# Kernel optimization log

Measured on AMD Instinct MI355X. Metric: run time of the kernel, lower is better.

Reference implementation:

```python
import jax, jax.numpy as jnp
import numpy as np

N_NODES = 50000
N_EDGES = 800000
NODE_FEAT = 3
EDGE_FEAT = 2
EMBED = 64
HIDDEN = 128
LAYERS = 4
POLY = 8


def setup_inputs() -> dict:
    key = jax.random.key(0)
    ks = jax.random.split(key, 24)
    s = 0.05
    inp = {
        "node_features": jax.random.normal(ks[0], (N_NODES, NODE_FEAT), jnp.float32),
        "edge_index": jax.random.randint(ks[1], (2, N_EDGES), 0, N_NODES, jnp.int32),
        "edge_features": jax.random.normal(ks[2], (N_EDGES, EDGE_FEAT), jnp.float32),
        "n": N_NODES,
        # node encoder MLP
        "enc_w1": jax.random.normal(ks[3], (NODE_FEAT, HIDDEN), jnp.float32) * s,
        "enc_b1": jnp.zeros((HIDDEN,), jnp.float32),
        "enc_w2": jax.random.normal(ks[4], (HIDDEN, EMBED), jnp.float32) * s,
        "enc_b2": jnp.zeros((EMBED,), jnp.float32),
        # per-layer conv message MLP (stacked over layers)
        "conv_w1": jax.random.normal(ks[5], (LAYERS, 2 * EMBED + EDGE_FEAT, EMBED), jnp.float32) * s,
        "conv_b1": jnp.zeros((LAYERS, EMBED), jnp.float32),
        "conv_w2": jax.random.normal(ks[6], (LAYERS, EMBED, EMBED), jnp.float32) * s,
        "conv_b2": jnp.zeros((LAYERS, EMBED), jnp.float32),
        # per-layer skip linear and layernorm
        "skip_w": jax.random.normal(ks[7], (LAYERS, EMBED, EMBED), jnp.float32) * s,
        "skip_b": jnp.zeros((LAYERS, EMBED), jnp.float32),
        "ln_g": jnp.ones((LAYERS, EMBED), jnp.float32),
        "ln_b": jnp.zeros((LAYERS, EMBED), jnp.float32),
        # polynomial head
        "head_w1": jax.random.normal(ks[8], (EMBED, EMBED), jnp.float32) * s,
        "head_b1": jnp.zeros((EMBED,), jnp.float32),
        "head_w2": jnp.zeros((EMBED, POLY), jnp.float32),  # zero-init per module
        "head_b2": jnp.ones((POLY,), jnp.float32),         # bias filled with 1.0
    }
    return inp


def _layernorm(x, g, b, eps=1e-5):
    mu = jnp.mean(x, axis=-1, keepdims=True)
    var = jnp.var(x, axis=-1, keepdims=True)
    return (x - mu) * jax.lax.rsqrt(var + eps) * g + b


def reference(node_features, edge_index, edge_features, n,
              enc_w1, enc_b1, enc_w2, enc_b2,
              conv_w1, conv_b1, conv_w2, conv_b2,
              skip_w, skip_b, ln_g, ln_b,
              head_w1, head_b1, head_w2, head_b2):
    rows, cols = edge_index[0], edge_index[1]
    # node encoder
    h = jax.nn.relu(node_features @ enc_w1 + enc_b1) @ enc_w2 + enc_b2  # [n, E]
    L = conv_w1.shape[0]
    for i in range(L):
        # gather + concat: [E_edges, 2*embed + edge_feat]
        msg_in = jnp.concatenate([h[rows], h[cols], edge_features], axis=-1)
        msg = jax.nn.relu(msg_in @ conv_w1[i] + conv_b1[i]) @ conv_w2[i] + conv_b2[i]
        agg = jax.ops.segment_sum(msg, rows, num_segments=n)  # scatter_add over source rows
        h_new = agg + h @ skip_w[i] + skip_b[i]
        h = jax.nn.relu(_layernorm(h_new, ln_g[i], ln_b[i]))
    # polynomial head
    return jax.nn.relu(h @ head_w1 + head_b1) @ head_w2 + head_b2  # [n, poly_degree]
```

## Files before the change

kernel.cpp:

```cpp
#include <hip/hip_runtime.h>

typedef unsigned short u16;
typedef __attribute__((ext_vector_type(8))) short bf16x8;
typedef __attribute__((ext_vector_type(4))) float f32x4;

#define MFMA16(a,b,c) __builtin_amdgcn_mfma_f32_16x16x32_bf16((a),(b),(c),0,0,0)

static __device__ __forceinline__ u16 f2bf(float x){
    unsigned int u = __float_as_uint(x);
    u += 0x7FFFu + ((u >> 16) & 1u);
    return (u16)(u >> 16);
}
static __device__ __forceinline__ float bf2f(short s){
    return __uint_as_float(((unsigned int)(u16)s) << 16);
}

static __device__ __forceinline__ bf16x8 load_bfrag(const float* __restrict__ W, int ldn, int n, int k0){
    bf16x8 r;
    #pragma unroll
    for (int j = 0; j < 8; ++j) r[j] = (short)f2bf(W[(k0 + j) * ldn + n]);
    return r;
}

__global__ __launch_bounds__(256) void enc_kernel(
    const float* __restrict__ X, const float* __restrict__ W1, const float* __restrict__ B1,
    const float* __restrict__ W2, const float* __restrict__ B2,
    const float* __restrict__ cW1, const float* __restrict__ cB1,
    u16* __restrict__ hbf, u16* __restrict__ Ubf, u16* __restrict__ Vbf, int N)
{
    __shared__ u16 sHid[64 * 136];
    __shared__ u16 sH[64 * 72];
    const int tid = threadIdx.x;
    const int w = tid >> 6, l = tid & 63, l15 = l & 15, quad = l >> 4;

    bf16x8 bW[4][4];
    #pragma unroll
    for (int ks = 0; ks < 4; ++ks)
        #pragma unroll
        for (int f = 0; f < 4; ++f)
            bW[ks][f] = load_bfrag(W2, 64, f * 16 + l15, ks * 32 + quad * 8);
    float b2v[4];
    #pragma unroll
    for (int f = 0; f < 4; ++f) b2v[f] = B2[f * 16 + l15];

    const int nbase = blockIdx.x * 64 + w * 16;

    {
        int e = l >> 2;
        int node = nbase + e; if (node > N - 1) node = N - 1;
        float x0 = X[node * 3], x1 = X[node * 3 + 1], x2 = X[node * 3 + 2];
        int k0 = (l & 3) * 32;
        u16* dst = sHid + (w * 16 + e) * 136 + k0;
        #pragma unroll
        for (int j = 0; j < 32; ++j){
            int k = k0 + j;
            float hv = x0 * W1[k] + x1 * W1[128 + k] + x2 * W1[256 + k] + B1[k];
            dst[j] = f2bf(hv > 0.f ? hv : 0.f);
        }
    }

    f32x4 acc[4];
    #pragma unroll
    for (int f = 0; f < 4; ++f){ acc[f][0]=b2v[f]; acc[f][1]=b2v[f]; acc[f][2]=b2v[f]; acc[f][3]=b2v[f]; }
    #pragma unroll
    for (int ks = 0; ks < 4; ++ks){
        bf16x8 a = *(const bf16x8*)&sHid[(w * 16 + l15) * 136 + ks * 32 + quad * 8];
        #pragma unroll
        for (int f = 0; f < 4; ++f) acc[f] = MFMA16(a, bW[ks][f], acc[f]);
    }
    #pragma unroll
    for (int r = 0; r < 4; ++r){
        int node = nbase + quad * 4 + r;
        #pragma unroll
        for (int f = 0; f < 4; ++f){
            u16 hb = f2bf(acc[f][r]);
            sH[(w * 16 + quad * 4 + r) * 72 + f * 16 + l15] = hb;
            if (node < N) hbf[(size_t)node * 64 + f * 16 + l15] = hb;
        }
    }

    bf16x8 bA[2][4], bB[2][4];
    #pragma unroll
    for (int kk = 0; kk < 2; ++kk)
        #pragma unroll
        for (int f = 0; f < 4; ++f){
            int n = f * 16 + l15, k0 = kk * 32 + quad * 8;
            bA[kk][f] = load_bfrag(cW1,           64, n, k0);
            bB[kk][f] = load_bfrag(cW1 + 64 * 64, 64, n, k0);
        }
    float b1n[4];
    #pragma unroll
    for (int f = 0; f < 4; ++f) b1n[f] = cB1[f * 16 + l15];

    bf16x8 a0 = *(const bf16x8*)&sH[(w * 16 + l15) * 72 + quad * 8];
    bf16x8 a1 = *(const bf16x8*)&sH[(w * 16 + l15) * 72 + 32 + quad * 8];

    f32x4 ua[4], va[4];
    #pragma unroll
    for (int f = 0; f < 4; ++f){
        ua[f][0]=b1n[f]; ua[f][1]=b1n[f]; ua[f][2]=b1n[f]; ua[f][3]=b1n[f];
        va[f][0]=0.f; va[f][1]=0.f; va[f][2]=0.f; va[f][3]=0.f;
    }
    #pragma unroll
    for (int f = 0; f < 4; ++f){ ua[f] = MFMA16(a0, bA[0][f], ua[f]); va[f] = MFMA16(a0, bB[0][f], va[f]); }
    #pragma unroll
    for (int f = 0; f < 4; ++f){ ua[f] = MFMA16(a1, bA[1][f], ua[f]); va[f] = MFMA16(a1, bB[1][f], va[f]); }

    #pragma unroll
    for (int r = 0; r < 4; ++r){
        int node = nbase + quad * 4 + r;
        if (node < N){
            #pragma unroll
            for (int f = 0; f < 4; ++f){
                Ubf[(size_t)node * 64 + f * 16 + l15] = f2bf(ua[f][r]);
                Vbf[(size_t)node * 64 + f * 16 + l15] = f2bf(va[f][r]);
            }
        }
    }
}

__global__ __launch_bounds__(256) void countB_kernel(const int* __restrict__ rows,
                                                     int* __restrict__ countsB, int E, int NB){
    __shared__ int c[1024];
    for (int i = threadIdx.x; i < NB; i += 256) c[i] = 0;
    __syncthreads();
    for (int i = blockIdx.x * 256 + threadIdx.x; i < E; i += gridDim.x * 256)
        atomicAdd(&c[rows[i] >> 6], 1);
    __syncthreads();
    for (int i = threadIdx.x; i < NB; i += 256){
        int v = c[i];
        if (v) atomicAdd(&countsB[i], v);
    }
}

__global__ __launch_bounds__(1024) void scanB_kernel(const int* __restrict__ countsB,
                                                     int* __restrict__ offsets,
                                                     int* __restrict__ cursorB, int NB){
    __shared__ int sc[1024];
    const int tid = threadIdx.x;
    int x = (tid < NB) ? countsB[tid] : 0;
    sc[tid] = x;
    __syncthreads();
    for (int d = 1; d < 1024; d <<= 1){
        int v = (tid >= d) ? sc[tid - d] : 0;
        __syncthreads();
        sc[tid] += v;
        __syncthreads();
    }
    int excl = sc[tid] - x;
    if (tid < NB){ offsets[tid] = excl; cursorB[tid] = excl; }
    if (tid == NB - 1) offsets[NB] = sc[tid];
}

#define CHUNK 8192

__global__ __launch_bounds__(1024) void binpack_kernel(
    const int* __restrict__ rows, const int* __restrict__ cols,
    const float* __restrict__ EF, int* __restrict__ cursorB,
    uint2* __restrict__ erec, int E)
{
    __shared__ u16 sRow[CHUNK];
    __shared__ u16 sPerm[CHUNK];
    __shared__ int cntA[1024], cntE[1024], cntC[1024], baseB[1024], sc[1024];
    const int tid = threadIdx.x;
    const int cbase = blockIdx.x * CHUNK;
    int C = E - cbase; if (C > CHUNK) C = CHUNK;
    if (C <= 0) return;

    cntA[tid] = 0;
    __syncthreads();
    for (int k = tid; k < C; k += 1024){
        int r = rows[cbase + k];
        sRow[k] = (u16)r;
        atomicAdd(&cntA[r >> 6], 1);
    }
    __syncthreads();
    sc[tid] = cntA[tid];
    __syncthreads();
    for (int d = 1; d < 1024; d <<= 1){
        int v = (tid >= d) ? sc[tid - d] : 0;
        __syncthreads();
        sc[tid] += v;
        __syncthreads();
    }
    int excl = sc[tid] - cntA[tid];
    cntE[tid] = excl;
    cntC[tid] = excl;
    if (cntA[tid] > 0) baseB[tid] = atomicAdd(&cursorB[tid], cntA[tid]);
    __syncthreads();
    for (int k = tid; k < C; k += 1024){
        int b = sRow[k] >> 6;
        int p = atomicAdd(&cntC[b], 1);
        sPerm[p] = (u16)k;
    }
    __syncthreads();
    for (int p = tid; p < C; p += 1024){
        int k = sPerm[p];
        int i = cbase + k;
        int r = sRow[k];
        int b = r >> 6;
        float2 ef = *(const float2*)&EF[2 * i];
        uint2 v;
        v.x = (unsigned)r | ((unsigned)cols[i] << 16);
        v.y = (unsigned)f2bf(ef.x) | ((unsigned)f2bf(ef.y) << 16);
        erec[baseB[b] + (p - cntE[b])] = v;
    }
}

#define ISSUE_UV(recv, U0, U1, V0, V1) do {                                  \
    int rr_ = (int)((recv).x & 0xFFFFu); if (rr_ == 0xFFFF) rr_ = 0;         \
    int cc_ = (int)((recv).x >> 16);                                         \
    const u16* pu_ = Ubf + (size_t)rr_ * 64 + quad * 8;                      \
    const u16* pv_ = Vbf + (size_t)cc_ * 64 + quad * 8;                      \
    U0 = *(const bf16x8*)(pu_);                                              \
    U1 = *(const bf16x8*)(pu_ + 32);                                         \
    V0 = *(const bf16x8*)(pv_);                                              \
    V1 = *(const bf16x8*)(pv_ + 32);                                         \
} while (0)

static __device__ __forceinline__ unsigned cvtpk(float a, float b){
    unsigned d;
    asm("v_cvt_pk_bf16_f32 %0, %1, %2" : "=v"(d) : "v"(a), "v"(b));
    return d;
}
#define PACK8(dst, x) do {                                                   \
    union { bf16x8 v; unsigned int d[4]; } _u;                               \
    _u.d[0] = cvtpk(x[0], x[1]); _u.d[1] = cvtpk(x[2], x[3]);                \
    _u.d[2] = cvtpk(x[4], x[5]); _u.d[3] = cvtpk(x[6], x[7]);                \
    dst = _u.v;                                                              \
} while (0)

__global__ __launch_bounds__(256, 3) void fused_kernel(
    const u16* __restrict__ Ubf, const u16* __restrict__ Vbf,
    const uint2* __restrict__ erec, const int* __restrict__ offsets,
    const float* __restrict__ W1,
    const float* __restrict__ W2, const float* __restrict__ B2,
    u16* __restrict__ hbf,
    const float* __restrict__ SW, const float* __restrict__ SB,
    const float* __restrict__ LG, const float* __restrict__ LB,
    const float* __restrict__ cW1, const float* __restrict__ cB1,
    u16* __restrict__ Un, u16* __restrict__ Vn,
    int N)
{
    __shared__ u16 sMsgT[2][64 * 72];
    __shared__ u16 sRowT[2][64];
    __shared__ u16 sH[64 * 72];
    const int tid = threadIdx.x;
    const int w = tid >> 6, l = tid & 63, l15 = l & 15, quad = l >> 4;
    const int w16 = w * 16;

    bf16x8 bW2[2][4];
    #pragma unroll
    for (int kk = 0; kk < 2; ++kk)
        #pragma unroll
        for (int f = 0; f < 4; ++f)
            bW2[kk][f] = load_bfrag(W2, 64, f * 16 + l15, kk * 32 + quad * 8);
    float bias2[4];
    #pragma unroll
    for (int f = 0; f < 4; ++f) bias2[f] = B2[f * 16 + l15];

    const float* Wc0 = W1 + 128 * 64;
    const float* Wc1 = W1 + 129 * 64;
    float e0l[8], e0h[8], e1l[8], e1h[8];
    #pragma unroll
    for (int j = 0; j < 8; ++j){
        int kl = quad * 8 + j;
        e0l[j] = Wc0[kl];       e0h[j] = Wc0[32 + kl];
        e1l[j] = Wc1[kl];       e1h[j] = Wc1[32 + kl];
    }

    const int b = blockIdx.x;
    const int start = offsets[b], end = offsets[b + 1];
    const int nt = (end - start + 63) >> 6;
    const int tgtrow = w16 + l15;

    f32x4 aggC[4] = {};

    auto LOADREC = [&](int t) -> uint2 {
        int e = start + t * 64 + w16 + l15;
        if (e < end) return erec[e];
        uint2 s; s.x = 0x0000FFFFu; s.y = 0u; return s;
    };

    if (nt > 0){
        uint2 recA = LOADREC(0);
        uint2 recB = (nt > 1) ? LOADREC(1) : recA;
        bf16x8 u0, u1, v0, v1;
        ISSUE_UV(recA, u0, u1, v0, v1);

        for (int t = 0; t < nt; ++t){
            uint2 recC = LOADREC(t + 2 < nt ? t + 2 : nt - 1);
            bf16x8 nu0, nu1, nv0, nv1;
            ISSUE_UV(recB, nu0, nu1, nv0, nv1);

            int rn_raw = (int)(recA.x & 0xFFFFu);
            float ef0 = bf2f((short)(recA.y & 0xFFFFu));
            float ef1 = bf2f((short)(recA.y >> 16));

            float xl[8], xh[8];
            #pragma unroll
            for (int j = 0; j < 8; ++j){
                float hA = fmaf(ef1, e1l[j], ef0 * e0l[j]);
                float hB = fmaf(ef1, e1h[j], ef0 * e0h[j]);
                xl[j] = fmaxf(hA + bf2f(u0[j]) + bf2f(v0[j]), 0.f);
                xh[j] = fmaxf(hB + bf2f(u1[j]) + bf2f(v1[j]), 0.f);
            }
            bf16x8 a0, a1;
            PACK8(a0, xl);
            PACK8(a1, xh);

            f32x4 m[4];
            #pragma unroll
            for (int f = 0; f < 4; ++f){ m[f][0]=bias2[f]; m[f][1]=bias2[f]; m[f][2]=bias2[f]; m[f][3]=bias2[f]; }
            #pragma unroll
            for (int f = 0; f < 4; ++f) m[f] = MFMA16(a0, bW2[0][f], m[f]);
            #pragma unroll
            for (int f = 0; f < 4; ++f) m[f] = MFMA16(a1, bW2[1][f], m[f]);

            const int buf = t & 1;
            #pragma unroll
            for (int f = 0; f < 4; ++f){
                uint2 wv;
                wv.x = cvtpk(m[f][0], m[f][1]);
                wv.y = cvtpk(m[f][2], m[f][3]);
                *(uint2*)&sMsgT[buf][(f * 16 + l15) * 72 + w16 + quad * 4] = wv;
            }
            if (quad == 0)
                sRowT[buf][w16 + l15] = (rn_raw == 0xFFFF) ? (u16)0xFFFF : (u16)(rn_raw & 63);

            __syncthreads();

            #pragma unroll
            for (int c = 0; c < 2; ++c){
                union { bf16x8 v; unsigned d[4]; } sfr;
                union { uint4 q; unsigned d[4]; } rv;
                rv.q = *(const uint4*)&sRowT[buf][c * 32 + quad * 8];
                #pragma unroll
                for (int k = 0; k < 4; ++k){
                    unsigned d = rv.d[k];
                    unsigned lo = d & 0xFFFFu, hi = d >> 16;
                    sfr.d[k] = (lo == (unsigned)tgtrow ? 0x3F80u : 0u)
                             | (hi == (unsigned)tgtrow ? 0x3F800000u : 0u);
                }
                #pragma unroll
                for (int f = 0; f < 4; ++f){
                    bf16x8 mb = *(const bf16x8*)&sMsgT[buf][(f * 16 + l15) * 72 + c * 32 + quad * 8];
                    aggC[f] = MFMA16(sfr.v, mb, aggC[f]);
                }
            }

            recA = recB; recB = recC;
            u0 = nu0; u1 = nu1; v0 = nv0; v1 = nv1;
        }
    }

    bf16x8 bW[2][4];
    #pragma unroll
    for (int kk = 0; kk < 2; ++kk)
        #pragma unroll
        for (int f = 0; f < 4; ++f)
            bW[kk][f] = load_bfrag(SW, 64, f * 16 + l15, kk * 32 + quad * 8);
    float sb[4], lg[4], lb[4];
    #pragma unroll
    for (int f = 0; f < 4; ++f){
        int n = f * 16 + l15;
        sb[f] = SB[n]; lg[f] = LG[n]; lb[f] = LB[n];
    }

    const int nbase = b * 64 + w16;
    int na = nbase + l15; if (na > N - 1) na = N - 1;
    const u16* pa = hbf + (size_t)na * 64 + quad * 8;
    bf16x8 h0 = *(const bf16x8*)pa;
    bf16x8 h1 = *(const bf16x8*)(pa + 32);

    f32x4 acc[4] = {};
    #pragma unroll
    for (int f = 0; f < 4; ++f) acc[f] = MFMA16(h0, bW[0][f], acc[f]);
    #pragma unroll
    for (int f = 0; f < 4; ++f) acc[f] = MFMA16(h1, bW[1][f], acc[f]);

    float vals[4][4];
    #pragma unroll
    for (int r = 0; r < 4; ++r)
        #pragma unroll
        for (int f = 0; f < 4; ++f)
            vals[f][r] = acc[f][r] + sb[f] + aggC[f][r];

    #pragma unroll
    for (int r = 0; r < 4; ++r){
        float s  = vals[0][r] + vals[1][r] + vals[2][r] + vals[3][r];
        float sq = vals[0][r]*vals[0][r] + vals[1][r]*vals[1][r]
                 + vals[2][r]*vals[2][r] + vals[3][r]*vals[3][r];
        #pragma unroll
        for (int msk = 1; msk < 16; msk <<= 1){
            s  += __shfl_xor(s,  msk);
            sq += __shfl_xor(sq, msk);
        }
        float mean = s * (1.f / 64.f);
        float var  = sq * (1.f / 64.f) - mean * mean;
        float rstd = rsqrtf(var + 1e-5f);
        int node = nbase + quad * 4 + r;
        #pragma unroll
        for (int f = 0; f < 4; ++f){
            float hv = (vals[f][r] - mean) * rstd * lg[f] + lb[f];
            hv = hv > 0.f ? hv : 0.f;
            u16 hb = f2bf(hv);
            sH[(w16 + quad * 4 + r) * 72 + f * 16 + l15] = hb;
            if (node < N) hbf[(size_t)node * 64 + f * 16 + l15] = hb;
        }
    }

    if (cW1){
        bf16x8 bA[2][4], bB[2][4];
        #pragma unroll
        for (int kk = 0; kk < 2; ++kk)
            #pragma unroll
            for (int f = 0; f < 4; ++f){
                int n = f * 16 + l15, k0 = kk * 32 + quad * 8;
                bA[kk][f] = load_bfrag(cW1,           64, n, k0);
                bB[kk][f] = load_bfrag(cW1 + 64 * 64, 64, n, k0);
            }
        float b1n[4];
        #pragma unroll
        for (int f = 0; f < 4; ++f) b1n[f] = cB1[f * 16 + l15];

        bf16x8 a0 = *(const bf16x8*)&sH[(w16 + l15) * 72 + quad * 8];
        bf16x8 a1 = *(const bf16x8*)&sH[(w16 + l15) * 72 + 32 + quad * 8];

        f32x4 ua[4], va[4];
        #pragma unroll
        for (int f = 0; f < 4; ++f){
            ua[f][0]=b1n[f]; ua[f][1]=b1n[f]; ua[f][2]=b1n[f]; ua[f][3]=b1n[f];
            va[f][0]=0.f; va[f][1]=0.f; va[f][2]=0.f; va[f][3]=0.f;
        }
        #pragma unroll
        for (int f = 0; f < 4; ++f){ ua[f] = MFMA16(a0, bA[0][f], ua[f]); va[f] = MFMA16(a0, bB[0][f], va[f]); }
        #pragma unroll
        for (int f = 0; f < 4; ++f){ ua[f] = MFMA16(a1, bA[1][f], ua[f]); va[f] = MFMA16(a1, bB[1][f], va[f]); }

        #pragma unroll
        for (int r = 0; r < 4; ++r){
            int node = nbase + quad * 4 + r;
            if (node < N){
                #pragma unroll
                for (int f = 0; f < 4; ++f){
                    Un[(size_t)node * 64 + f * 16 + l15] = f2bf(ua[f][r]);
                    Vn[(size_t)node * 64 + f * 16 + l15] = f2bf(va[f][r]);
                }
            }
        }
    }
}

__global__ __launch_bounds__(256) void head_kernel(
    const u16* __restrict__ hbf,
    const float* __restrict__ W1, const float* __restrict__ B1,
    const float* __restrict__ W2, const float* __restrict__ B2,
    float* __restrict__ out, int N)
{
    __shared__ u16 sT[64 * 72];
    const int tid = threadIdx.x;
    const int w = tid >> 6, l = tid & 63, l15 = l & 15, quad = l >> 4;

    bf16x8 bW1[2][4];
    #pragma unroll
    for (int kk = 0; kk < 2; ++kk)
        #pragma unroll
        for (int f = 0; f < 4; ++f)
            bW1[kk][f] = load_bfrag(W1, 64, f * 16 + l15, kk * 32 + quad * 8);
    float b1v[4];
    #pragma unroll
    for (int f = 0; f < 4; ++f) b1v[f] = B1[f * 16 + l15];

    bf16x8 bW2[2];
    #pragma unroll
    for (int kk = 0; kk < 2; ++kk)
        #pragma unroll
        for (int j = 0; j < 8; ++j){
            int k = kk * 32 + quad * 8 + j;
            bW2[kk][j] = (l15 < 8) ? (short)f2bf(W2[k * 8 + l15]) : (short)0;
        }
    float b2v = (l15 < 8) ? B2[l15] : 0.f;

    const int nbase = blockIdx.x * 64 + w * 16;
    int na = nbase + l15; if (na > N - 1) na = N - 1;
    const u16* pa = hbf + (size_t)na * 64 + quad * 8;
    bf16x8 a0 = *(const bf16x8*)pa;
    bf16x8 a1 = *(const bf16x8*)(pa + 32);

    f32x4 acc[4];
    #pragma unroll
    for (int f = 0; f < 4; ++f){ acc[f][0]=b1v[f]; acc[f][1]=b1v[f]; acc[f][2]=b1v[f]; acc[f][3]=b1v[f]; }
    #pragma unroll
    for (int f = 0; f < 4; ++f) acc[f] = MFMA16(a0, bW1[0][f], acc[f]);
    #pragma unroll
    for (int f = 0; f < 4; ++f) acc[f] = MFMA16(a1, bW1[1][f], acc[f]);

    u16* myT = sT + (w * 16) * 72;
    #pragma unroll
    for (int f = 0; f < 4; ++f)
        #pragma unroll
        for (int r = 0; r < 4; ++r){
            float v = acc[f][r] > 0.f ? acc[f][r] : 0.f;
            myT[(quad * 4 + r) * 72 + f * 16 + l15] = f2bf(v);
        }

    f32x4 o = { b2v, b2v, b2v, b2v };
    #pragma unroll
    for (int kk = 0; kk < 2; ++kk){
        bf16x8 a = *(const bf16x8*)&myT[l15 * 72 + kk * 32 + quad * 8];
        o = MFMA16(a, bW2[kk], o);
    }
    #pragma unroll
    for (int r = 0; r < 4; ++r){
        int node = nbase + quad * 4 + r;
        if (node < N && l15 < 8)
            out[(size_t)node * 8 + l15] = o[r];
    }
}

extern "C" void kernel_launch(void* const* d_in, const int* in_sizes, int n_in,
                              void* d_out, int out_size, void* d_ws, size_t ws_size,
                              hipStream_t stream)
{
    const float* X      = (const float*)d_in[0];
    const int*   EI     = (const int*)d_in[1];
    const float* EF     = (const float*)d_in[2];
    const float* encW1  = (const float*)d_in[4];
    const float* encB1  = (const float*)d_in[5];
    const float* encW2  = (const float*)d_in[6];
    const float* encB2  = (const float*)d_in[7];
    const float* convW1 = (const float*)d_in[8];
    const float* convB1 = (const float*)d_in[9];
    const float* convW2 = (const float*)d_in[10];
    const float* convB2 = (const float*)d_in[11];
    const float* skipW  = (const float*)d_in[12];
    const float* skipB  = (const float*)d_in[13];
    const float* lnG    = (const float*)d_in[14];
    const float* lnB    = (const float*)d_in[15];
    const float* headW1 = (const float*)d_in[16];
    const float* headB1 = (const float*)d_in[17];
    const float* headW2 = (const float*)d_in[18];
    const float* headB2 = (const float*)d_in[19];

    const int N = in_sizes[0] / 3;
    const int E = in_sizes[1] / 2;
    const int L = in_sizes[8] / (130 * 64);
    const int* rows = EI;
    const int* cols = EI + E;

    const int NB = (N + 63) / 64;

    auto align256 = [](size_t x){ return (x + 255) & ~(size_t)255; };
    char* p = (char*)d_ws;
    u16* hbf   = (u16*)p;           p += align256((size_t)N * 64 * 2);
    u16* Ubuf0 = (u16*)p;           p += align256((size_t)N * 64 * 2);
    u16* Vbuf0 = (u16*)p;           p += align256((size_t)N * 64 * 2);
    u16* Ubuf1 = (u16*)p;           p += align256((size_t)N * 64 * 2);
    u16* Vbuf1 = (u16*)p;           p += align256((size_t)N * 64 * 2);
    uint2* erec = (uint2*)p;        p += align256((size_t)E * 8);
    int* countsB = (int*)p;         p += align256(1024 * 4);
    int* offsets = (int*)p;         p += align256(1032 * 4);
    int* cursorB = (int*)p;         p += align256(1024 * 4);

    hipMemsetAsync(countsB, 0, (size_t)NB * sizeof(int), stream);
    countB_kernel<<<256, 256, 0, stream>>>(rows, countsB, E, NB);
    scanB_kernel<<<1, 1024, 0, stream>>>(countsB, offsets, cursorB, NB);
    binpack_kernel<<<(E + CHUNK - 1) / CHUNK, 1024, 0, stream>>>(rows, cols, EF, cursorB, erec, E);

    enc_kernel<<<NB, 256, 0, stream>>>(X, encW1, encB1, encW2, encB2,
                                       convW1, convB1, hbf, Ubuf0, Vbuf0, N);

    u16* Ucur = Ubuf0; u16* Vcur = Vbuf0;
    u16* Ualt = Ubuf1; u16* Valt = Vbuf1;
    for (int li = 0; li < L; ++li){
        const float* w1n = (li + 1 < L) ? convW1 + (size_t)(li + 1) * 130 * 64 : nullptr;
        const float* b1n = (li + 1 < L) ? convB1 + (li + 1) * 64 : nullptr;
        fused_kernel<<<NB, 256, 0, stream>>>(Ucur, Vcur, erec, offsets,
            convW1 + (size_t)li * 130 * 64,
            convW2 + (size_t)li * 64 * 64, convB2 + li * 64,
            hbf,
            skipW + (size_t)li * 64 * 64, skipB + li * 64,
            lnG + li * 64, lnB + li * 64,
            w1n, b1n, Ualt, Valt, N);
        u16* t;
        t = Ucur; Ucur = Ualt; Ualt = t;
        t = Vcur; Vcur = Valt; Valt = t;
    }
    head_kernel<<<NB, 256, 0, stream>>>(hbf, headW1, headB1, headW2, headB2,
                                        (float*)d_out, N);
}
```

Baseline: 327.1 us.

## Shrink fused-layer node blocks from 64 to 48 rows for more blocks

Changes the node bucketing from 64-row to 48-row blocks, using a multiply-shift divide-by-48, so the fused per-layer kernel launches about 1042 blocks instead of 782. This should spread work more evenly across the GPU's compute units. Supporting this meant rewriting the scan kernels to handle more than 1024 buckets with wave-shuffle scans, and only 3 of 4 waves now run the skip/layernorm epilogue. It also stores the edge-feature weight columns as bf16 packs to cut register use, which adds small rounding error. The extra block count costs some additional weight loading per block and leaves one wave idle in the epilogue.

```diff
diff --git a/kernel.cpp b/kernel.cpp
--- a/kernel.cpp
+++ b/kernel.cpp
@@ -5,6 +5,7 @@
 typedef __attribute__((ext_vector_type(4))) float f32x4;
 
 #define MFMA16(a,b,c) __builtin_amdgcn_mfma_f32_16x16x32_bf16((a),(b),(c),0,0,0)
+#define BROW 48
 
 static __device__ __forceinline__ u16 f2bf(float x){
     unsigned int u = __float_as_uint(x);
@@ -14,6 +15,7 @@
 static __device__ __forceinline__ float bf2f(short s){
     return __uint_as_float(((unsigned int)(u16)s) << 16);
 }
+static __device__ __forceinline__ int div48(int r){ return ((r >> 4) * 43691) >> 17; }
 
 static __device__ __forceinline__ bf16x8 load_bfrag(const float* __restrict__ W, int ldn, int n, int k0){
     bf16x8 r;
@@ -121,11 +123,11 @@
 
 __global__ __launch_bounds__(256) void countB_kernel(const int* __restrict__ rows,
                                                      int* __restrict__ countsB, int E, int NB){
-    __shared__ int c[1024];
-    for (int i = threadIdx.x; i < NB; i += 256) c[i] = 0;
+    __shared__ int c[2048];
+    for (int i = threadIdx.x; i < 2048; i += 256) c[i] = 0;
     __syncthreads();
     for (int i = blockIdx.x * 256 + threadIdx.x; i < E; i += gridDim.x * 256)
-        atomicAdd(&c[rows[i] >> 6], 1);
+        atomicAdd(&c[div48(rows[i])], 1);
     __syncthreads();
     for (int i = threadIdx.x; i < NB; i += 256){
         int v = c[i];
@@ -135,21 +137,41 @@
 
 __global__ __launch_bounds__(1024) void scanB_kernel(const int* __restrict__ countsB,
                                                      int* __restrict__ offsets,
-                                                     int* __restrict__ cursorB, int NB){
-    __shared__ int sc[1024];
-    const int tid = threadIdx.x;
-    int x = (tid < NB) ? countsB[tid] : 0;
-    sc[tid] = x;
-    __syncthreads();
-    for (int d = 1; d < 1024; d <<= 1){
-        int v = (tid >= d) ? sc[tid - d] : 0;
+                                                     int* __restrict__ cursorB, int n)
+{
+    __shared__ int wsum[16];
+    __shared__ int carry_s;
+    const int tid = threadIdx.x, lane = tid & 63, wv = tid >> 6;
+    if (tid == 0) carry_s = 0;
+    __syncthreads();
+    for (int base = 0; base < n; base += 1024){
+        int i = base + tid;
+        int x = (i < n) ? countsB[i] : 0;
+        int inc = x;
+        #pragma unroll
+        for (int d = 1; d < 64; d <<= 1){
+            int t = __shfl_up(inc, d);
+            if (lane >= d) inc += t;
+        }
+        if (lane == 63) wsum[wv] = inc;
         __syncthreads();
-        sc[tid] += v;
+        if (tid < 16){
+            int s = wsum[tid], si = s;
+            #pragma unroll
+            for (int d = 1; d < 16; d <<= 1){
+                int t = __shfl_up(si, d);
+                if (tid >= d) si += t;
+            }
+            wsum[tid] = si - s;
+        }
         __syncthreads();
-    }
-    int excl = sc[tid] - x;
-    if (tid < NB){ offsets[tid] = excl; cursorB[tid] = excl; }
-    if (tid == NB - 1) offsets[NB] = sc[tid];
+        int excl = inc - x + wsum[wv] + carry_s;
+        if (i < n){ offsets[i] = excl; cursorB[i] = excl; }
+        if (i == n - 1) offsets[n] = excl + x;
+        __syncthreads();
+        if (tid == 1023) carry_s += wsum[15] + inc;
+        __syncthreads();
+    }
 }
 
 #define CHUNK 8192
@@ -161,36 +183,53 @@
 {
     __shared__ u16 sRow[CHUNK];
     __shared__ u16 sPerm[CHUNK];
-    __shared__ int cntA[1024], cntE[1024], cntC[1024], baseB[1024], sc[1024];
-    const int tid = threadIdx.x;
+    __shared__ int cntA[2048];
+    __shared__ int cntC[2048];
+    __shared__ int baseB[2048];
+    __shared__ u16 cntE[2048];
+    __shared__ int wsum[16];
+    const int tid = threadIdx.x, lane = tid & 63, wv = tid >> 6;
     const int cbase = blockIdx.x * CHUNK;
     int C = E - cbase; if (C > CHUNK) C = CHUNK;
     if (C <= 0) return;
 
-    cntA[tid] = 0;
+    cntA[tid] = 0; cntA[tid + 1024] = 0;
     __syncthreads();
     for (int k = tid; k < C; k += 1024){
         int r = rows[cbase + k];
         sRow[k] = (u16)r;
-        atomicAdd(&cntA[r >> 6], 1);
-    }
-    __syncthreads();
-    sc[tid] = cntA[tid];
-    __syncthreads();
-    for (int d = 1; d < 1024; d <<= 1){
-        int v = (tid >= d) ? sc[tid - d] : 0;
-        __syncthreads();
-        sc[tid] += v;
-        __syncthreads();
-    }
-    int excl = sc[tid] - cntA[tid];
-    cntE[tid] = excl;
-    cntC[tid] = excl;
-    if (cntA[tid] > 0) baseB[tid] = atomicAdd(&cursorB[tid], cntA[tid]);
+        atomicAdd(&cntA[div48(r)], 1);
+    }
+    __syncthreads();
+    int a = cntA[2 * tid], bq = cntA[2 * tid + 1];
+    int x = a + bq;
+    int inc = x;
+    #pragma unroll
+    for (int d = 1; d < 64; d <<= 1){
+        int t = __shfl_up(inc, d);
+        if (lane >= d) inc += t;
+    }
+    if (lane == 63) wsum[wv] = inc;
+    __syncthreads();
+    if (tid < 16){
+        int s = wsum[tid], si = s;
+        #pragma unroll
+        for (int d = 1; d < 16; d <<= 1){
+            int t = __shfl_up(si, d);
+            if (tid >= d) si += t;
+        }
+        wsum[tid] = si - s;
+    }
+    __syncthreads();
+    int excl = inc - x + wsum[wv];
+    cntE[2 * tid] = (u16)excl;       cntE[2 * tid + 1] = (u16)(excl + a);
+    cntC[2 * tid] = excl;            cntC[2 * tid + 1] = excl + a;
+    if (a  > 0) baseB[2 * tid]     = atomicAdd(&cursorB[2 * tid],     a);
+    if (bq > 0) baseB[2 * tid + 1] = atomicAdd(&cursorB[2 * tid + 1], bq);
     __syncthreads();
     for (int k = tid; k < C; k += 1024){
-        int b = sRow[k] >> 6;
-        int p = atomicAdd(&cntC[b], 1);
+        int bk = div48((int)sRow[k]);
+        int p = atomicAdd(&cntC[bk], 1);
         sPerm[p] = (u16)k;
     }
     __syncthreads();
@@ -198,12 +237,12 @@
         int k = sPerm[p];
         int i = cbase + k;
         int r = sRow[k];
-        int b = r >> 6;
+        int bk = div48(r);
         float2 ef = *(const float2*)&EF[2 * i];
         uint2 v;
         v.x = (unsigned)r | ((unsigned)cols[i] << 16);
         v.y = (unsigned)f2bf(ef.x) | ((unsigned)f2bf(ef.y) << 16);
-        erec[baseB[b] + (p - cntE[b])] = v;
+        erec[baseB[bk] + (p - (int)cntE[bk])] = v;
     }
 }
 
@@ -261,17 +300,18 @@
 
     const float* Wc0 = W1 + 128 * 64;
     const float* Wc1 = W1 + 129 * 64;
-    float e0l[8], e0h[8], e1l[8], e1h[8];
+    bf16x8 e0lo, e0hi, e1lo, e1hi;
     #pragma unroll
     for (int j = 0; j < 8; ++j){
         int kl = quad * 8 + j;
-        e0l[j] = Wc0[kl];       e0h[j] = Wc0[32 + kl];
-        e1l[j] = Wc1[kl];       e1h[j] = Wc1[32 + kl];
+        e0lo[j] = (short)f2bf(Wc0[kl]);      e0hi[j] = (short)f2bf(Wc0[32 + kl]);
+        e1lo[j] = (short)f2bf(Wc1[kl]);      e1hi[j] = (short)f2bf(Wc1[32 + kl]);
     }
 
     const int b = blockIdx.x;
     const int start = offsets[b], end = offsets[b + 1];
     const int nt = (end - start + 63) >> 6;
+    const int rowbase = b * BROW;
     const int tgtrow = w16 + l15;
 
     f32x4 aggC[4] = {};
@@ -300,8 +340,8 @@
             float xl[8], xh[8];
             #pragma unroll
             for (int j = 0; j < 8; ++j){
-                float hA = fmaf(ef1, e1l[j], ef0 * e0l[j]);
-                float hB = fmaf(ef1, e1h[j], ef0 * e0h[j]);
+                float hA = fmaf(ef1, bf2f(e1lo[j]), ef0 * bf2f(e0lo[j]));
+                float hB = fmaf(ef1, bf2f(e1hi[j]), ef0 * bf2f(e0hi[j]));
                 xl[j] = fmaxf(hA + bf2f(u0[j]) + bf2f(v0[j]), 0.f);
                 xh[j] = fmaxf(hB + bf2f(u1[j]) + bf2f(v1[j]), 0.f);
             }
@@ -326,7 +366,8 @@
                 *(uint2*)&sMsgT[buf][(f * 16 + l15) * 72 + w16 + quad * 4] = wv;
             }
             if (quad == 0)
-                sRowT[buf][w16 + l15] = (rn_raw == 0xFFFF) ? (u16)0xFFFF : (u16)(rn_raw & 63);
+                sRowT[buf][w16 + l15] = (rn_raw == 0xFFFF) ? (u16)0xFFFF
+                                                           : (u16)(rn_raw - rowbase);
 
             __syncthreads();
 
@@ -354,98 +395,102 @@
         }
     }
 
-    bf16x8 bW[2][4];
-    #pragma unroll
-    for (int kk = 0; kk < 2; ++kk)
-        #pragma unroll
-        for (int f = 0; f < 4; ++f)
-            bW[kk][f] = load_bfrag(SW, 64, f * 16 + l15, kk * 32 + quad * 8);
-    float sb[4], lg[4], lb[4];
-    #pragma unroll
-    for (int f = 0; f < 4; ++f){
-        int n = f * 16 + l15;
-        sb[f] = SB[n]; lg[f] = LG[n]; lb[f] = LB[n];
-    }
-
-    const int nbase = b * 64 + w16;
-    int na = nbase + l15; if (na > N - 1) na = N - 1;
-    const u16* pa = hbf + (size_t)na * 64 + quad * 8;
-    bf16x8 h0 = *(const bf16x8*)pa;
-    bf16x8 h1 = *(const bf16x8*)(pa + 32);
-
-    f32x4 acc[4] = {};
-    #pragma unroll
-    for (int f = 0; f < 4; ++f) acc[f] = MFMA16(h0, bW[0][f], acc[f]);
-    #pragma unroll
-    for (int f = 0; f < 4; ++f) acc[f] = MFMA16(h1, bW[1][f], acc[f]);
-
-    float vals[4][4];
-    #pragma unroll
-    for (int r = 0; r < 4; ++r)
-        #pragma unroll
-        for (int f = 0; f < 4; ++f)
-            vals[f][r] = acc[f][r] + sb[f] + aggC[f][r];
-
-    #pragma unroll
-    for (int r = 0; r < 4; ++r){
-        float s  = vals[0][r] + vals[1][r] + vals[2][r] + vals[3][r];
-        float sq = vals[0][r]*vals[0][r] + vals[1][r]*vals[1][r]
-                 + vals[2][r]*vals[2][r] + vals[3][r]*vals[3][r];
-        #pragma unroll
-        for (int msk = 1; msk < 16; msk <<= 1){
-            s  += __shfl_xor(s,  msk);
-            sq += __shfl_xor(sq, msk);
-        }
-        float mean = s * (1.f / 64.f);
-        float var  = sq * (1.f / 64.f) - mean * mean;
-        float rstd = rsqrtf(var + 1e-5f);
-        int node = nbase + quad * 4 + r;
+    __syncthreads();
+
+    if (w < 3){
+        bf16x8 bW[2][4];
+        #pragma unroll
+        for (int kk = 0; kk < 2; ++kk)
+            #pragma unroll
+            for (int f = 0; f < 4; ++f)
+                bW[kk][f] = load_bfrag(SW, 64, f * 16 + l15, kk * 32 + quad * 8);
+        float sb[4], lg[4], lb[4];
         #pragma unroll
         for (int f = 0; f < 4; ++f){
-            float hv = (vals[f][r] - mean) * rstd * lg[f] + lb[f];
-            hv = hv > 0.f ? hv : 0.f;
-            u16 hb = f2bf(hv);
-            sH[(w16 + quad * 4 + r) * 72 + f * 16 + l15] = hb;
-            if (node < N) hbf[(size_t)node * 64 + f * 16 + l15] = hb;
-        }
-    }
-
-    if (cW1){
-        bf16x8 bA[2][4], bB[2][4];
-        #pragma unroll
-        for (int kk = 0; kk < 2; ++kk)
+            int n = f * 16 + l15;
+            sb[f] = SB[n]; lg[f] = LG[n]; lb[f] = LB[n];
+        }
+
+        const int nbase = rowbase + w16;
+        int na = nbase + l15; if (na > N - 1) na = N - 1;
+        const u16* pa = hbf + (size_t)na * 64 + quad * 8;
+        bf16x8 h0 = *(const bf16x8*)pa;
+        bf16x8 h1 = *(const bf16x8*)(pa + 32);
+
+        f32x4 acc[4] = {};
+        #pragma unroll
+        for (int f = 0; f < 4; ++f) acc[f] = MFMA16(h0, bW[0][f], acc[f]);
+        #pragma unroll
+        for (int f = 0; f < 4; ++f) acc[f] = MFMA16(h1, bW[1][f], acc[f]);
+
+        float vals[4][4];
+        #pragma unroll
+        for (int r = 0; r < 4; ++r)
+            #pragma unroll
+            for (int f = 0; f < 4; ++f)
+                vals[f][r] = acc[f][r] + sb[f] + aggC[f][r];
+
+        #pragma unroll
+        for (int r = 0; r < 4; ++r){
+            float s  = vals[0][r] + vals[1][r] + vals[2][r] + vals[3][r];
+            float sq = vals[0][r]*vals[0][r] + vals[1][r]*vals[1][r]
+                     + vals[2][r]*vals[2][r] + vals[3][r]*vals[3][r];
+            #pragma unroll
+            for (int msk = 1; msk < 16; msk <<= 1){
+                s  += __shfl_xor(s,  msk);
+                sq += __shfl_xor(sq, msk);
+            }
+            float mean = s * (1.f / 64.f);
+            float var  = sq * (1.f / 64.f) - mean * mean;
+            float rstd = rsqrtf(var + 1e-5f);
+            int node = nbase + quad * 4 + r;
             #pragma unroll
             for (int f = 0; f < 4; ++f){
-                int n = f * 16 + l15, k0 = kk * 32 + quad * 8;
-                bA[kk][f] = load_bfrag(cW1,           64, n, k0);
-                bB[kk][f] = load_bfrag(cW1 + 64 * 64, 64, n, k0);
-            }
-        float b1n[4];
-        #pragma unroll
-        for (int f = 0; f < 4; ++f) b1n[f] = cB1[f * 16 + l15];
-
-        bf16x8 a0 = *(const bf16x8*)&sH[(w16 + l15) * 72 + quad * 8];
-        bf16x8 a1 = *(const bf16x8*)&sH[(w16 + l15) * 72 + 32 + quad * 8];
-
-        f32x4 ua[4], va[4];
-        #pragma unroll
-        for (int f = 0; f < 4; ++f){
-            ua[f][0]=b1n[f]; ua[f][1]=b1n[f]; ua[f][2]=b1n[f]; ua[f][3]=b1n[f];
-            va[f][0]=0.f; va[f][1]=0.f; va[f][2]=0.f; va[f][3]=0.f;
-        }
-        #pragma unroll
-        for (int f = 0; f < 4; ++f){ ua[f] = MFMA16(a0, bA[0][f], ua[f]); va[f] = MFMA16(a0, bB[0][f], va[f]); }
-        #pragma unroll
-        for (int f = 0; f < 4; ++f){ ua[f] = MFMA16(a1, bA[1][f], ua[f]); va[f] = MFMA16(a1, bB[1][f], va[f]); }
-
-        #pragma unroll
-        for (int r = 0; r < 4; ++r){
-            int node = nbase + quad * 4 + r;
-            if (node < N){
+                float hv = (vals[f][r] - mean) * rstd * lg[f] + lb[f];
+                hv = hv > 0.f ? hv : 0.f;
+                u16 hb = f2bf(hv);
+                sH[(w16 + quad * 4 + r) * 72 + f * 16 + l15] = hb;
+                if (node < N) hbf[(size_t)node * 64 + f * 16 + l15] = hb;
+            }
+        }
+
+        if (cW1){
+            bf16x8 bA[2][4], bB[2][4];
+            #pragma unroll
+            for (int kk = 0; kk < 2; ++kk)
                 #pragma unroll
                 for (int f = 0; f < 4; ++f){
-                    Un[(size_t)node * 64 + f * 16 + l15] = f2bf(ua[f][r]);
-                    Vn[(size_t)node * 64 + f * 16 + l15] = f2bf(va[f][r]);
+                    int n = f * 16 + l15, k0 = kk * 32 + quad * 8;
+                    bA[kk][f] = load_bfrag(cW1,           64, n, k0);
+                    bB[kk][f] = load_bfrag(cW1 + 64 * 64, 64, n, k0);
+                }
+            float b1n[4];
+            #pragma unroll
+            for (int f = 0; f < 4; ++f) b1n[f] = cB1[f * 16 + l15];
+
+            bf16x8 a0 = *(const bf16x8*)&sH[(w16 + l15) * 72 + quad * 8];
+            bf16x8 a1 = *(const bf16x8*)&sH[(w16 + l15) * 72 + 32 + quad * 8];
+
+            f32x4 ua[4], va[4];
+            #pragma unroll
+            for (int f = 0; f < 4; ++f){
+                ua[f][0]=b1n[f]; ua[f][1]=b1n[f]; ua[f][2]=b1n[f]; ua[f][3]=b1n[f];
+                va[f][0]=0.f; va[f][1]=0.f; va[f][2]=0.f; va[f][3]=0.f;
+            }
+            #pragma unroll
+            for (int f = 0; f < 4; ++f){ ua[f] = MFMA16(a0, bA[0][f], ua[f]); va[f] = MFMA16(a0, bB[0][f], va[f]); }
+            #pragma unroll
+            for (int f = 0; f < 4; ++f){ ua[f] = MFMA16(a1, bA[1][f], ua[f]); va[f] = MFMA16(a1, bB[1][f], va[f]); }
+
+            #pragma unroll
+            for (int r = 0; r < 4; ++r){
+                int node = nbase + quad * 4 + r;
+                if (node < N){
+                    #pragma unroll
+                    for (int f = 0; f < 4; ++f){
+                        Un[(size_t)node * 64 + f * 16 + l15] = f2bf(ua[f][r]);
+                        Vn[(size_t)node * 64 + f * 16 + l15] = f2bf(va[f][r]);
+                    }
                 }
             }
         }
@@ -549,7 +594,8 @@
     const int* rows = EI;
     const int* cols = EI + E;
 
-    const int NB = (N + 63) / 64;
+    const int NB64 = (N + 63) / 64;
+    const int NB48 = (N + 47) / 48;
 
     auto align256 = [](size_t x){ return (x + 255) & ~(size_t)255; };
     char* p = (char*)d_ws;
@@ -559,24 +605,24 @@
     u16* Ubuf1 = (u16*)p;           p += align256((size_t)N * 64 * 2);
     u16* Vbuf1 = (u16*)p;           p += align256((size_t)N * 64 * 2);
     uint2* erec = (uint2*)p;        p += align256((size_t)E * 8);
-    int* countsB = (int*)p;         p += align256(1024 * 4);
-    int* offsets = (int*)p;         p += align256(1032 * 4);
-    int* cursorB = (int*)p;         p += align256(1024 * 4);
-
-    hipMemsetAsync(countsB, 0, (size_t)NB * sizeof(int), stream);
-    countB_kernel<<<256, 256, 0, stream>>>(rows, countsB, E, NB);
-    scanB_kernel<<<1, 1024, 0, stream>>>(countsB, offsets, cursorB, NB);
+    int* countsB = (int*)p;         p += align256(2048 * 4);
+    int* offsets = (int*)p;         p += align256(2056 * 4);
+    int* cursorB = (int*)p;         p += align256(2048 * 4);
+
+    hipMemsetAsync(countsB, 0, (size_t)NB48 * sizeof(int), stream);
+    countB_kernel<<<256, 256, 0, stream>>>(rows, countsB, E, NB48);
+    scanB_kernel<<<1, 1024, 0, stream>>>(countsB, offsets, cursorB, NB48);
     binpack_kernel<<<(E + CHUNK - 1) / CHUNK, 1024, 0, stream>>>(rows, cols, EF, cursorB, erec, E);
 
-    enc_kernel<<<NB, 256, 0, stream>>>(X, encW1, encB1, encW2, encB2,
-                                       convW1, convB1, hbf, Ubuf0, Vbuf0, N);
+    enc_kernel<<<NB64, 256, 0, stream>>>(X, encW1, encB1, encW2, encB2,
+                                         convW1, convB1, hbf, Ubuf0, Vbuf0, N);
 
     u16* Ucur = Ubuf0; u16* Vcur = Vbuf0;
     u16* Ualt = Ubuf1; u16* Valt = Vbuf1;
     for (int li = 0; li < L; ++li){
         const float* w1n = (li + 1 < L) ? convW1 + (size_t)(li + 1) * 130 * 64 : nullptr;
         const float* b1n = (li + 1 < L) ? convB1 + (li + 1) * 64 : nullptr;
-        fused_kernel<<<NB, 256, 0, stream>>>(Ucur, Vcur, erec, offsets,
+        fused_kernel<<<NB48, 256, 0, stream>>>(Ucur, Vcur, erec, offsets,
             convW1 + (size_t)li * 130 * 64,
             convW2 + (size_t)li * 64 * 64, convB2 + li * 64,
             hbf,
@@ -587,6 +633,6 @@
         t = Ucur; Ucur = Ualt; Ualt = t;
         t = Vcur; Vcur = Valt; Valt = t;
     }
-    head_kernel<<<NB, 256, 0, stream>>>(hbf, headW1, headB1, headW2, headB2,
-                                        (float*)d_out, N);
-}
+    head_kernel<<<NB64, 256, 0, stream>>>(hbf, headW1, headB1, headW2, headB2,
+                                          (float*)d_out, N);
+}
```

Measured after the change: 306.7 us (median of 2 runs). -6.2%, faster.
